# Performance work log

Hardware: AMD Instinct MI355X
Metric: run time of the kernel (lower is better)

Reference implementation:

```python
import jax, jax.numpy as jnp
import numpy as np


def _propagate(x, src, dst, norm, n):
    # PyG propagate with aggr='add': out[dst_e] += norm_e * x[src_e]
    return jax.ops.segment_sum(x[src] * norm[:, None], dst, num_segments=n)


def _dconv(x, w, b, row, col, norm_out, norm_in, n):
    # DConv with K=2: w has shape (2, 2, c_in, c_out)
    # k=0 term: identity for both diffusion directions
    h = x @ w[0, 0] + x @ w[1, 0]
    # k=1 term: 1-hop diffusion, forward edges and flipped edges
    tx_o = _propagate(x, row, col, norm_out, n)  # out-degree normalized walk
    tx_i = _propagate(x, col, row, norm_in, n)   # edge_index.flip([0]) walk
    h = h + tx_o @ w[0, 1] + tx_i @ w[1, 1]
    return h + b


def reference(x, edge_index, edge_weight, w_lin2, b_lin2, w_z, b_z, w_r, b_r, w_h, b_h, w_out, b_out):
    n = x.shape[0]
    row, col = edge_index[0], edge_index[1]
    # degrees from weighted adjacency (same as to_dense_adj row/col sums)
    deg_out = jax.ops.segment_sum(edge_weight, row, num_segments=n)
    deg_in = jax.ops.segment_sum(edge_weight, col, num_segments=n)
    norm_out = (1.0 / deg_out)[row]
    norm_in = (1.0 / deg_in)[row]

    h = x.reshape(n, -1)                      # Flatten: (n, 24)
    h = jax.nn.sigmoid(h @ w_lin2 + b_lin2)   # (n, hidden)

    # DCRNN GRU cell, hidden state initialized to zeros (single step)
    h0 = jnp.zeros_like(h)
    xh = jnp.concatenate([h, h0], axis=1)     # (n, 2*hidden)
    z = jax.nn.sigmoid(_dconv(xh, w_z, b_z, row, col, norm_out, norm_in, n))
    r = jax.nn.sigmoid(_dconv(xh, w_r, b_r, row, col, norm_out, norm_in, n))
    xhr = jnp.concatenate([h, h0 * r], axis=1)
    h_tilde = jnp.tanh(_dconv(xhr, w_h, b_h, row, col, norm_out, norm_in, n))
    h_new = z * h0 + (1.0 - z) * h_tilde

    return jax.nn.sigmoid(h_new) @ w_out + b_out  # (n, out_periods)


def setup_inputs() -> dict:
    key = jax.random.key(0)
    ks = jax.random.split(key, 12)
    N, DEG, HID, OUTP, WIN, HOR = 100000, 8, 64, 12, 2, 12
    E = N * DEG

    x = jax.random.normal(ks[0], (N, WIN, HOR), dtype=jnp.float32)

    # random edges + a ring so every node has out-degree>=1 and in-degree>=1
    e_rand = N * (DEG - 1)
    row_r = jax.random.randint(ks[1], (e_rand,), 0, N, dtype=jnp.int32)
    col_r = jax.random.randint(ks[2], (e_rand,), 0, N, dtype=jnp.int32)
    ring = jnp.arange(N, dtype=jnp.int32)
    row = jnp.concatenate([row_r, ring])
    col = jnp.concatenate([col_r, (ring + 1) % N])
    edge_index = jnp.stack([row, col])  # (2, E)
    edge_weight = jax.random.uniform(ks[3], (E,), minval=0.5, maxval=1.5, dtype=jnp.float32)

    def lin_w(k, fi, fo):
        return jax.random.normal(k, (fi, fo), jnp.float32) / np.float32(np.sqrt(fi))

    def dconv_w(k, cin, cout):
        return jax.random.normal(k, (2, 2, cin, cout), jnp.float32) / np.float32(np.sqrt(cin))

    cin = 2 * HID
    return {
        "x": x,
        "edge_index": edge_index,
        "edge_weight": edge_weight,
        "w_lin2": lin_w(ks[4], WIN * HOR, HID),
        "b_lin2": jnp.zeros((HID,), jnp.float32),
        "w_z": dconv_w(ks[5], cin, HID),
        "b_z": jnp.zeros((HID,), jnp.float32),
        "w_r": dconv_w(ks[6], cin, HID),
        "b_r": jnp.zeros((HID,), jnp.float32),
        "w_h": dconv_w(ks[7], cin, HID),
        "b_h": jnp.zeros((HID,), jnp.float32),
        "w_out": lin_w(ks[8], HID, OUTP),
        "b_out": jnp.zeros((OUTP,), jnp.float32),
    }
```

## Files before the change

kernel.cpp:

```cpp
#include <hip/hip_runtime.h>


typedef unsigned long long ull;
typedef unsigned short ushort;
typedef unsigned int uint;
typedef __attribute__((ext_vector_type(8))) short bf16x8;
typedef __attribute__((ext_vector_type(4))) float f32x4;

#define BSZ    64
#define CAP    768
#define CHUNK  4096
#define MAXBKT 2048

__device__ __forceinline__ float sigmoid_f(float x) {
    return 1.0f / (1.0f + __expf(-x));
}
__device__ __forceinline__ float tanh_f(float x) {
    float ax = fabsf(x);
    float e = __expf(-2.0f * ax);
    float t = (1.0f - e) / (1.0f + e);
    return copysignf(t, x);
}
__device__ __forceinline__ ushort f2bf(float f) {
    unsigned u = __float_as_uint(f);
    return (ushort)((u + 0x7FFF + ((u >> 16) & 1)) >> 16);
}
__device__ __forceinline__ float bf2f(ushort s) {
    return __uint_as_float(((unsigned)s) << 16);
}

__global__ void init_kernel(uint* __restrict__ gcur, int nbkt) {
    int t = blockIdx.x * 1024 + threadIdx.x;
    if (t < 2 * nbkt) gcur[t] = (uint)(t % nbkt) * CAP;
}

__global__ void __launch_bounds__(256) mega1_kernel(
        const int* __restrict__ row, const int* __restrict__ col,
        const float* __restrict__ ew, int E,
        uint* __restrict__ gcur, ull* __restrict__ pkbuf,
        int nbkt, int nslot,
        const float* __restrict__ x, const float* __restrict__ Wl,
        const float* __restrict__ bl, ushort* __restrict__ hb, int N,
        const float* __restrict__ wz, const float* __restrict__ bz,
        const float* __restrict__ wh, const float* __restrict__ bh,
        ushort* __restrict__ Wp, float* __restrict__ bc, int SB, int LB) {
    __shared__ float Ws[24 * 64];
    __shared__ float bs[64];
    __shared__ uint hist[2 * MAXBKT];
    __shared__ uint base_s[2 * MAXBKT];
    int bx = blockIdx.x;
    const int t = threadIdx.x;

    if (bx < SB) {
        int e0 = bx * CHUNK;
        for (int i = t; i < 2 * nbkt; i += 256) hist[i] = 0;
        __syncthreads();
#pragma unroll
        for (int j = 0; j < CHUNK / 256; ++j) {
            int e = e0 + j * 256 + t;
            if (e < E) {
                atomicAdd(&hist[col[e] >> 6], 1u);
                atomicAdd(&hist[nbkt + (row[e] >> 6)], 1u);
            }
        }
        __syncthreads();
        for (int i = t; i < 2 * nbkt; i += 256) {
            uint c = hist[i];
            base_s[i] = c ? atomicAdd(&gcur[i], c) : 0u;
            hist[i] = 0;
        }
        __syncthreads();
#pragma unroll
        for (int j = 0; j < CHUNK / 256; ++j) {
            int e = e0 + j * 256 + t;
            if (e < E) {
                int r0 = row[e], c0 = col[e];
                uint w15 = (uint)(ew[e] * 16384.0f + 0.5f);
                int b0 = c0 >> 6;
                uint s0 = base_s[b0] + atomicAdd(&hist[b0], 1u);
                if (s0 < ((uint)b0 + 1u) * CAP)
                    pkbuf[s0] = ((ull)(uint)r0 << 32) |
                                ((uint)(c0 & (BSZ - 1)) << 15) | w15;
                int b1 = nbkt + (r0 >> 6);
                uint s1 = base_s[b1] + atomicAdd(&hist[b1], 1u);
                if (s1 < ((uint)(r0 >> 6) + 1u) * CAP)
                    pkbuf[(size_t)nslot + s1] = ((ull)(uint)c0 << 32) |
                                ((uint)(r0 & (BSZ - 1)) << 15) | w15;
            }
        }
        return;
    }
    bx -= SB;
    if (bx < LB) {
        for (int i = t; i < 384; i += 256)
            ((float4*)Ws)[i] = ((const float4*)Wl)[i];
        if (t < 64) bs[t] = bl[t];
        __syncthreads();
        int gid = bx * 256 + t;
        int n = gid >> 6;
        int c = gid & 63;
        if (n >= N) return;
        const float* xr = x + (size_t)n * 24;
        float acc = bs[c];
#pragma unroll
        for (int k4 = 0; k4 < 6; ++k4) {
            float4 xv = *(const float4*)(xr + k4 * 4);
            acc = fmaf(xv.x, Ws[(k4 * 4 + 0) * 64 + c], acc);
            acc = fmaf(xv.y, Ws[(k4 * 4 + 1) * 64 + c], acc);
            acc = fmaf(xv.z, Ws[(k4 * 4 + 2) * 64 + c], acc);
            acc = fmaf(xv.w, Ws[(k4 * 4 + 3) * 64 + c], acc);
        }
        hb[(size_t)n * 64 + c] = f2bf(sigmoid_f(acc));
        return;
    }
    bx -= LB;
    int i = bx * 256 + t;
    if (bx == 0 && t < 128) bc[t] = (t < 64) ? bz[t] : bh[t - 64];
    if (i >= 6 * 8 * 64 * 8) return;
    int j    = i & 7;
    int lane = (i >> 3) & 63;
    int ct   = (i >> 9) & 7;
    int kt   = i >> 12;
    int k = kt * 32 + 8 * (lane >> 4) + j;
    int c = ct * 16 + (lane & 15);
    const float* w = (c < 64) ? wz : wh;
    int cc = c & 63;
    float v;
    if (k < 64)        v = w[(0 * 128 + k) * 64 + cc] + w[(2 * 128 + k) * 64 + cc];
    else if (k < 128)  v = w[(1 * 128 + (k - 64)) * 64 + cc];
    else               v = w[(3 * 128 + (k - 128)) * 64 + cc];
    Wp[i] = f2bf(v);
}

__global__ void __launch_bounds__(256) sort_kernel(
        const uint* __restrict__ gcur, const ull* __restrict__ pkbuf,
        uint* __restrict__ srt, int* __restrict__ beg, int* __restrict__ end,
        float* __restrict__ rdi, float* __restrict__ rdo,
        int nbkt, int nslot, int N) {
    __shared__ uint hist[BSZ];
    __shared__ uint pre[BSZ];
    __shared__ uint cur[BSZ];
    __shared__ float sdeg[BSZ];
    const int b = blockIdx.x, d = blockIdx.y, t = threadIdx.x;
    if (t < BSZ) { hist[t] = 0; sdeg[t] = 0.0f; }
    __syncthreads();
    uint cnt = gcur[d * nbkt + b] - (uint)b * CAP;
    if (cnt > CAP) cnt = CAP;
    const ull* rec = pkbuf + (size_t)d * nslot + (size_t)b * CAP;
    for (uint i = t; i < cnt; i += 256) {
        ull r = rec[i];
        uint dl = (uint)(r >> 15) & (BSZ - 1);
        atomicAdd(&hist[dl], 1u);
        atomicAdd(&sdeg[dl], (float)(uint)(r & 0x7FFFu));
    }
    __syncthreads();
    if (t < BSZ) {
        int v = (int)hist[t];
        int x = v;
#pragma unroll
        for (int off = 1; off < BSZ; off <<= 1) {
            int y = __shfl_up(x, off, 64);
            if (t >= off) x += y;
        }
        uint p = (uint)(x - v);
        pre[t] = p;
        cur[t] = p;
        int n = b * BSZ + t;
        if (n < N) {
            beg[(size_t)d * N + n] = (int)((uint)b * CAP + p);
            end[(size_t)d * N + n] = (int)((uint)b * CAP + p + (uint)v);
            float s = sdeg[t];
            float rv = (s > 0.0f) ? (16384.0f / s) : 0.0f;
            if (d == 0) rdi[n] = rv;
            else        rdo[n] = rv;
        }
    }
    __syncthreads();
    uint* so = srt + (size_t)d * nslot + (size_t)b * CAP;
    for (uint i = t; i < cnt; i += 256) {
        ull r = rec[i];
        uint dl = (uint)(r >> 15) & (BSZ - 1);
        uint p = atomicAdd(&cur[dl], 1u);
        so[p] = (uint)(r >> 32);
    }
}

__global__ void __launch_bounds__(256) gather_kernel(
        const ushort* __restrict__ hb, const uint* __restrict__ srt,
        const int* __restrict__ beg, const int* __restrict__ end,
        const float* __restrict__ rdo, const float* __restrict__ rdi,
        ushort* __restrict__ pob, ushort* __restrict__ pib,
        int nslot, int N) {
    int n = blockIdx.x * 4 + (threadIdx.x >> 6);
    if (n >= N) return;
    int lane = threadIdx.x & 63;
    int d = blockIdx.y;
    const uint* s_ = srt + (size_t)d * nslot;
    int s0 = beg[(size_t)d * N + n];
    int s1 = end[(size_t)d * N + n];

    if (d == 0) {
        float acc = 0.0f;
        for (int s = s0; s < s1; s += 8) {
            int m = s1 - s;
            int idx[8];
#pragma unroll
            for (int j = 0; j < 8; ++j) idx[j] = (int)s_[(s + j < s1) ? s + j : s1 - 1];
            float w[8];
#pragma unroll
            for (int j = 0; j < 8; ++j) w[j] = (j < m) ? rdo[idx[j]] : 0.0f;
            float v[8];
#pragma unroll
            for (int j = 0; j < 8; ++j) v[j] = bf2f(hb[(size_t)idx[j] * 64 + lane]);
#pragma unroll
            for (int j = 0; j < 8; ++j) acc = fmaf(v[j], w[j], acc);
        }
        pob[(size_t)n * 64 + lane] = f2bf(acc);
    } else {
        float acc = 0.0f;
        for (int s = s0; s < s1; s += 8) {
            int m = s1 - s;
            int idx[8];
#pragma unroll
            for (int j = 0; j < 8; ++j) idx[j] = (int)s_[(s + j < s1) ? s + j : s1 - 1];
            float v[8];
#pragma unroll
            for (int j = 0; j < 8; ++j) v[j] = bf2f(hb[(size_t)idx[j] * 64 + lane]);
#pragma unroll
            for (int j = 0; j < 8; ++j) acc += (j < m) ? v[j] : 0.0f;
        }
        pib[(size_t)n * 64 + lane] = f2bf(acc * rdi[n]);
    }
}

__global__ void __launch_bounds__(256) gates_kernel(
        const ushort* __restrict__ hb, const ushort* __restrict__ pob,
        const ushort* __restrict__ pib, const ushort* __restrict__ Wp,
        const float* __restrict__ bc, const float* __restrict__ wout,
        const float* __restrict__ bout, float* __restrict__ out, int N) {
    __shared__ float sS[64 * 68];
    __shared__ float sWO[64 * 12];
    const int t    = threadIdx.x;
    const int w    = t >> 6;
    const int lane = t & 63;
    const int n0   = blockIdx.x * 64;

    for (int i = t; i < 64 * 12; i += 256) sWO[i] = wout[i];

    f32x4 acc[8];
#pragma unroll
    for (int ct = 0; ct < 8; ++ct) {
        float bcv = bc[ct * 16 + (lane & 15)];
        acc[ct] = (f32x4){bcv, bcv, bcv, bcv};
    }

    int arow = n0 + w * 16 + (lane & 15);
    if (arow >= N) arow = N - 1;
    const int g8 = (lane >> 4) * 8;
    const ushort* const srcs[3] = {hb, pob, pib};

#pragma unroll
    for (int kc = 0; kc < 6; ++kc) {
        const ushort* src = srcs[kc >> 1];
        bf16x8 a = *(const bf16x8*)(src + (size_t)arow * 64 + (kc & 1) * 32 + g8);
#pragma unroll
        for (int ct = 0; ct < 8; ++ct) {
            bf16x8 b = *(const bf16x8*)(Wp + (size_t)((kc * 8 + ct) * 64 + lane) * 8);
            acc[ct] = __builtin_amdgcn_mfma_f32_16x16x32_bf16(a, b, acc[ct], 0, 0, 0);
        }
    }

    const int rowbase = w * 16 + (lane >> 4) * 4;
    const int colbase = lane & 15;
#pragma unroll
    for (int ct = 0; ct < 4; ++ct) {
#pragma unroll
        for (int r = 0; r < 4; ++r) {
            float zv = sigmoid_f(acc[ct][r]);
            float ht = tanh_f(acc[ct + 4][r]);
            sS[(rowbase + r) * 68 + ct * 16 + colbase] =
                sigmoid_f((1.0f - zv) * ht);
        }
    }
    __syncthreads();

#pragma unroll
    for (int rr = 0; rr < 3; ++rr) {
        int o = rr * 256 + t;
        int node = o / 12;
        int j = o % 12;
        int n = n0 + node;
        if (n >= N) continue;
        float a = bout[j];
#pragma unroll 8
        for (int c2 = 0; c2 < 64; ++c2) a = fmaf(sS[node * 68 + c2], sWO[c2 * 12 + j], a);
        out[(size_t)n * 12 + j] = a;
    }
}

extern "C" void kernel_launch(void* const* d_in, const int* in_sizes, int n_in,
                              void* d_out, int out_size, void* d_ws, size_t ws_size,
                              hipStream_t stream) {
    const float* x      = (const float*)d_in[0];
    const int*   ei     = (const int*)  d_in[1];
    const float* ew     = (const float*)d_in[2];
    const float* w_lin2 = (const float*)d_in[3];
    const float* b_lin2 = (const float*)d_in[4];
    const float* w_z    = (const float*)d_in[5];
    const float* b_z    = (const float*)d_in[6];
    const float* w_h    = (const float*)d_in[9];
    const float* b_h    = (const float*)d_in[10];
    const float* w_out  = (const float*)d_in[11];
    const float* b_out  = (const float*)d_in[12];

    int N = in_sizes[0] / 24;
    int E = in_sizes[1] / 2;
    const int* row = ei;
    const int* col = ei + E;
    int nbkt  = (N + BSZ - 1) / BSZ;
    int nslot = nbkt * CAP;

    ull*    pkbuf = (ull*)d_ws;
    uint*   srt   = (uint*)(pkbuf + 2 * (size_t)nslot);
    ushort* hb    = (ushort*)(srt + 2 * (size_t)nslot);
    ushort* pob   = hb  + (size_t)N * 64;
    ushort* pib   = pob + (size_t)N * 64;
    ushort* Wp    = pib + (size_t)N * 64;
    float*  bc    = (float*)(Wp + 24576);
    float*  rdo   = bc + 128;
    float*  rdi   = rdo + N;
    int*    beg   = (int*)(rdi + N);
    int*    end   = beg + 2 * (size_t)N;
    uint*   gcur  = (uint*)(end + 2 * (size_t)N);

    int SB = (E + CHUNK - 1) / CHUNK;
    int LB = (N * 64 + 255) / 256;
    int PB = (6 * 8 * 64 * 8 + 255) / 256;

    init_kernel<<<(2 * nbkt + 1023) / 1024, 1024, 0, stream>>>(gcur, nbkt);
    mega1_kernel<<<SB + LB + PB, 256, 0, stream>>>(
        row, col, ew, E, gcur, pkbuf, nbkt, nslot,
        x, w_lin2, b_lin2, hb, N,
        w_z, b_z, w_h, b_h, Wp, bc, SB, LB);
    sort_kernel<<<dim3(nbkt, 2), 256, 0, stream>>>(gcur, pkbuf, srt, beg, end,
                                                   rdi, rdo, nbkt, nslot, N);
    gather_kernel<<<dim3((N + 3) / 4, 2), 256, 0, stream>>>(hb, srt, beg, end,
                                                            rdo, rdi, pob, pib,
                                                            nslot, N);
    gates_kernel<<<(N + 63) / 64, 256, 0, stream>>>(hb, pob, pib, Wp, bc,
                                                    w_out, b_out, (float*)d_out, N);
}
```

Before: 177.8 us.

## Split edge bucketing per direction and vectorize neighbor gather across lane groups

The edge bucketing blocks now handle one direction each, so twice as many blocks run with half the shared histogram. This should raise occupancy and halve the shared-memory atomic work per block, at the cost of reading each edge chunk twice. The gather kernel now has each wavefront load 4 bf16 features per lane (8-byte loads) for 4 neighbors in parallel and reduce across lane groups with shuffles. This replaces 64 scalar 2-byte loads per neighbor, aiming for wider memory transactions and more neighbors in flight. The unused prefix array in the sort kernel is also removed.

```diff
diff --git a/kernel.cpp b/kernel.cpp
--- a/kernel.cpp
+++ b/kernel.cpp
@@ -46,46 +46,42 @@
         ushort* __restrict__ Wp, float* __restrict__ bc, int SB, int LB) {
     __shared__ float Ws[24 * 64];
     __shared__ float bs[64];
-    __shared__ uint hist[2 * MAXBKT];
-    __shared__ uint base_s[2 * MAXBKT];
+    __shared__ uint hist[MAXBKT];
+    __shared__ uint base_s[MAXBKT];
     int bx = blockIdx.x;
     const int t = threadIdx.x;
 
     if (bx < SB) {
-        int e0 = bx * CHUNK;
-        for (int i = t; i < 2 * nbkt; i += 256) hist[i] = 0;
+        const int d  = bx & 1;
+        const int e0 = (bx >> 1) * CHUNK;
+        const int* key = d ? row : col;
+        const int* oth = d ? col : row;
+        for (int i = t; i < nbkt; i += 256) hist[i] = 0;
+        __syncthreads();
+#pragma unroll
+        for (int j = 0; j < CHUNK / 256; ++j) {
+            int e = e0 + j * 256 + t;
+            if (e < E) atomicAdd(&hist[key[e] >> 6], 1u);
+        }
+        __syncthreads();
+        for (int i = t; i < nbkt; i += 256) {
+            uint c = hist[i];
+            base_s[i] = c ? atomicAdd(&gcur[d * nbkt + i], c) : 0u;
+            hist[i] = 0;
+        }
         __syncthreads();
 #pragma unroll
         for (int j = 0; j < CHUNK / 256; ++j) {
             int e = e0 + j * 256 + t;
             if (e < E) {
-                atomicAdd(&hist[col[e] >> 6], 1u);
-                atomicAdd(&hist[nbkt + (row[e] >> 6)], 1u);
-            }
-        }
-        __syncthreads();
-        for (int i = t; i < 2 * nbkt; i += 256) {
-            uint c = hist[i];
-            base_s[i] = c ? atomicAdd(&gcur[i], c) : 0u;
-            hist[i] = 0;
-        }
-        __syncthreads();
-#pragma unroll
-        for (int j = 0; j < CHUNK / 256; ++j) {
-            int e = e0 + j * 256 + t;
-            if (e < E) {
-                int r0 = row[e], c0 = col[e];
+                int k   = key[e];
+                int bkt = k >> 6;
                 uint w15 = (uint)(ew[e] * 16384.0f + 0.5f);
-                int b0 = c0 >> 6;
-                uint s0 = base_s[b0] + atomicAdd(&hist[b0], 1u);
-                if (s0 < ((uint)b0 + 1u) * CAP)
-                    pkbuf[s0] = ((ull)(uint)r0 << 32) |
-                                ((uint)(c0 & (BSZ - 1)) << 15) | w15;
-                int b1 = nbkt + (r0 >> 6);
-                uint s1 = base_s[b1] + atomicAdd(&hist[b1], 1u);
-                if (s1 < ((uint)(r0 >> 6) + 1u) * CAP)
-                    pkbuf[(size_t)nslot + s1] = ((ull)(uint)c0 << 32) |
-                                ((uint)(r0 & (BSZ - 1)) << 15) | w15;
+                uint s = base_s[bkt] + atomicAdd(&hist[bkt], 1u);
+                if (s < ((uint)bkt + 1u) * CAP)
+                    pkbuf[(size_t)d * nslot + s] =
+                        ((ull)(uint)oth[e] << 32) |
+                        ((uint)(k & (BSZ - 1)) << 15) | w15;
             }
         }
         return;
@@ -138,7 +134,6 @@
         float* __restrict__ rdi, float* __restrict__ rdo,
         int nbkt, int nslot, int N) {
     __shared__ uint hist[BSZ];
-    __shared__ uint pre[BSZ];
     __shared__ uint cur[BSZ];
     __shared__ float sdeg[BSZ];
     const int b = blockIdx.x, d = blockIdx.y, t = threadIdx.x;
@@ -163,7 +158,6 @@
             if (t >= off) x += y;
         }
         uint p = (uint)(x - v);
-        pre[t] = p;
         cur[t] = p;
         int n = b * BSZ + t;
         if (n < N) {
@@ -193,43 +187,49 @@
         int nslot, int N) {
     int n = blockIdx.x * 4 + (threadIdx.x >> 6);
     if (n >= N) return;
-    int lane = threadIdx.x & 63;
-    int d = blockIdx.y;
+    const int lane = threadIdx.x & 63;
+    const int g    = lane >> 4;
+    const int cq   = (lane & 15) * 4;
+    const int d    = blockIdx.y;
     const uint* s_ = srt + (size_t)d * nslot;
     int s0 = beg[(size_t)d * N + n];
     int s1 = end[(size_t)d * N + n];
 
-    if (d == 0) {
-        float acc = 0.0f;
-        for (int s = s0; s < s1; s += 8) {
-            int m = s1 - s;
-            int idx[8];
-#pragma unroll
-            for (int j = 0; j < 8; ++j) idx[j] = (int)s_[(s + j < s1) ? s + j : s1 - 1];
-            float w[8];
-#pragma unroll
-            for (int j = 0; j < 8; ++j) w[j] = (j < m) ? rdo[idx[j]] : 0.0f;
-            float v[8];
-#pragma unroll
-            for (int j = 0; j < 8; ++j) v[j] = bf2f(hb[(size_t)idx[j] * 64 + lane]);
-#pragma unroll
-            for (int j = 0; j < 8; ++j) acc = fmaf(v[j], w[j], acc);
-        }
-        pob[(size_t)n * 64 + lane] = f2bf(acc);
-    } else {
-        float acc = 0.0f;
-        for (int s = s0; s < s1; s += 8) {
-            int m = s1 - s;
-            int idx[8];
-#pragma unroll
-            for (int j = 0; j < 8; ++j) idx[j] = (int)s_[(s + j < s1) ? s + j : s1 - 1];
-            float v[8];
-#pragma unroll
-            for (int j = 0; j < 8; ++j) v[j] = bf2f(hb[(size_t)idx[j] * 64 + lane]);
-#pragma unroll
-            for (int j = 0; j < 8; ++j) acc += (j < m) ? v[j] : 0.0f;
-        }
-        pib[(size_t)n * 64 + lane] = f2bf(acc * rdi[n]);
+    float a0 = 0.f, a1 = 0.f, a2 = 0.f, a3 = 0.f;
+    for (int s = s0; s < s1; s += 8) {
+        int sa = s + g, sb = s + 4 + g;
+        int ia = (int)s_[(sa < s1) ? sa : s1 - 1];
+        int ib = (int)s_[(sb < s1) ? sb : s1 - 1];
+        float wa, wb;
+        if (d == 0) {
+            wa = (sa < s1) ? rdo[ia] : 0.0f;
+            wb = (sb < s1) ? rdo[ib] : 0.0f;
+        } else {
+            wa = (sa < s1) ? 1.0f : 0.0f;
+            wb = (sb < s1) ? 1.0f : 0.0f;
+        }
+        uint2 ha = *(const uint2*)(hb + (size_t)ia * 64 + cq);
+        uint2 hc = *(const uint2*)(hb + (size_t)ib * 64 + cq);
+        a0 = fmaf(__uint_as_float(ha.x << 16),         wa, a0);
+        a1 = fmaf(__uint_as_float(ha.x & 0xFFFF0000u), wa, a1);
+        a2 = fmaf(__uint_as_float(ha.y << 16),         wa, a2);
+        a3 = fmaf(__uint_as_float(ha.y & 0xFFFF0000u), wa, a3);
+        a0 = fmaf(__uint_as_float(hc.x << 16),         wb, a0);
+        a1 = fmaf(__uint_as_float(hc.x & 0xFFFF0000u), wb, a1);
+        a2 = fmaf(__uint_as_float(hc.y << 16),         wb, a2);
+        a3 = fmaf(__uint_as_float(hc.y & 0xFFFF0000u), wb, a3);
+    }
+    a0 += __shfl_xor(a0, 16, 64); a0 += __shfl_xor(a0, 32, 64);
+    a1 += __shfl_xor(a1, 16, 64); a1 += __shfl_xor(a1, 32, 64);
+    a2 += __shfl_xor(a2, 16, 64); a2 += __shfl_xor(a2, 32, 64);
+    a3 += __shfl_xor(a3, 16, 64); a3 += __shfl_xor(a3, 32, 64);
+
+    if (lane < 16) {
+        float m = (d == 0) ? 1.0f : rdi[n];
+        uint lo = (uint)f2bf(a0 * m) | ((uint)f2bf(a1 * m) << 16);
+        uint hi = (uint)f2bf(a2 * m) | ((uint)f2bf(a3 * m) << 16);
+        ushort* dst = (d == 0 ? pob : pib) + (size_t)n * 64 + cq;
+        *(uint2*)dst = make_uint2(lo, hi);
     }
 }
 
@@ -333,7 +333,7 @@
     int*    end   = beg + 2 * (size_t)N;
     uint*   gcur  = (uint*)(end + 2 * (size_t)N);
 
-    int SB = (E + CHUNK - 1) / CHUNK;
+    int SB = 2 * ((E + CHUNK - 1) / CHUNK);
     int LB = (N * 64 + 255) / 256;
     int PB = (6 * 8 * 64 * 8 + 255) / 256;
 
```

New measurement: 164.8 us. 1.08x faster.
